# Kernel optimization log

Hardware: AMD Instinct MI355X
Metric: run time of the kernel (lower is better)

The kernel has to match this reference:

```python
import jax, jax.numpy as jnp
import numpy as np

N_NODES = 50000


def gcn_conv(x, W, b, src, dst, n):
    """PyG GCNConv: add self-loops, symmetric deg^-1/2 normalization, then aggregate."""
    loop = jnp.arange(n, dtype=src.dtype)
    s = jnp.concatenate([src, loop])  # [E+N]
    d = jnp.concatenate([dst, loop])  # [E+N]
    deg = jax.ops.segment_sum(jnp.ones_like(d, dtype=x.dtype), d, num_segments=n)  # [N]
    dinv = jnp.where(deg > 0, jax.lax.rsqrt(deg), 0.0)
    h = x @ W  # transform first (reduces message width), [N, out]
    norm = (dinv[s] * dinv[d])[:, None]  # [E+N, 1]
    msgs = h[s] * norm  # gather + scale, [E+N, out]
    out = jax.ops.segment_sum(msgs, d, num_segments=n)  # scatter-add, [N, out]
    return out + b


def setup_inputs() -> dict:
    key = jax.random.key(0)
    k1, k2, k3, k4 = jax.random.split(key, 4)
    in_dim, hidden, n_cls = 512, 256, 64
    x = jax.random.normal(k1, (N_NODES, in_dim), dtype=jnp.float32)
    edge_index = jax.random.randint(k2, (2, 800000), 0, N_NODES, dtype=jnp.int64)
    W1 = jax.random.normal(k3, (in_dim, hidden), dtype=jnp.float32) / np.sqrt(in_dim)
    b1 = jnp.zeros((hidden,), dtype=jnp.float32)
    W2 = jax.random.normal(k4, (hidden, n_cls), dtype=jnp.float32) / np.sqrt(hidden)
    b2 = jnp.zeros((n_cls,), dtype=jnp.float32)
    return {"x": x, "edge_index": edge_index, "W1": W1, "b1": b1, "W2": W2, "b2": b2}


def reference(x, edge_index, W1, b1, W2, b2):
    src, dst = edge_index[0], edge_index[1]
    n = x.shape[0]
    h = jax.nn.relu(gcn_conv(x, W1, b1, src, dst, n))  # dropout is identity in eval mode
    logits = gcn_conv(h, W2, b2, src, dst, n)
    evidence = jax.nn.softplus(logits)
    return (evidence, h)
```

## Files before the change

### kernel.cpp

```cpp
#include <hip/hip_runtime.h>


#define N_NODES 50000
#define IN_DIM 512
#define HID 256
#define NCLS 64

typedef unsigned short u16;
typedef unsigned int u32;
typedef __attribute__((ext_vector_type(8))) short short8;
typedef __attribute__((ext_vector_type(4))) float float4_t;

__device__ __forceinline__ float bf_lo(u32 v) {
    u32 u = v << 16; float f; __builtin_memcpy(&f, &u, 4); return f;
}
__device__ __forceinline__ float bf_hi(u32 v) {
    u32 u = v & 0xffff0000u; float f; __builtin_memcpy(&f, &u, 4); return f;
}
__device__ __forceinline__ u16 f2bf(float f) {
    u32 u; __builtin_memcpy(&u, &f, 4);
    return (u16)((u + 0x7fffu + ((u >> 16) & 1u)) >> 16);
}
__device__ __forceinline__ u32 pk_bf16(float lo, float hi) {
    u32 r;
    asm("v_cvt_pk_bf16_f32 %0, %1, %2" : "=v"(r) : "v"(lo), "v"(hi));
    return r;
}
__device__ __forceinline__ void add8(float* acc, uint4 v) {
    acc[0] += bf_lo(v.x); acc[1] += bf_hi(v.x);
    acc[2] += bf_lo(v.y); acc[3] += bf_hi(v.y);
    acc[4] += bf_lo(v.z); acc[5] += bf_hi(v.z);
    acc[6] += bf_lo(v.w); acc[7] += bf_hi(v.w);
}
__device__ __forceinline__ void acc8(float* acc, uint4 v, float w) {
    acc[0] += w * bf_lo(v.x); acc[1] += w * bf_hi(v.x);
    acc[2] += w * bf_lo(v.y); acc[3] += w * bf_hi(v.y);
    acc[4] += w * bf_lo(v.z); acc[5] += w * bf_hi(v.z);
    acc[6] += w * bf_lo(v.w); acc[7] += w * bf_hi(v.w);
}
__device__ __forceinline__ void nt_store4(float* p, float a, float b, float c, float d) {
    float4_t v = {a, b, c, d};
    __builtin_nontemporal_store(v, (float4_t*)p);
}

__global__ void init_kernel(int* __restrict__ cnt, int* __restrict__ cursor, int n) {
    int i = blockIdx.x * blockDim.x + threadIdx.x;
    if (i < n) { cnt[i] = 0; cursor[i] = 0; }
}

__global__ void count_kernel(const int* __restrict__ dst, int* __restrict__ cnt, int E) {
    int e = blockIdx.x * blockDim.x + threadIdx.x;
    if (e < E) atomicAdd(&cnt[dst[e]], 1);
}

__global__ __launch_bounds__(256) void s1_kernel(const int* __restrict__ cnt,
                                                 int* __restrict__ blocksum,
                                                 float* __restrict__ dinv, int n) {
    int tid = threadIdx.x;
    int i = blockIdx.x * 256 + tid;
    int c = (i < n) ? cnt[i] : 0;
    if (i < n) dinv[i] = rsqrtf((float)(c + 1));
    __shared__ int s[256];
    s[tid] = c;
    __syncthreads();
    for (int off = 128; off > 0; off >>= 1) {
        if (tid < off) s[tid] += s[tid + off];
        __syncthreads();
    }
    if (tid == 0) blocksum[blockIdx.x] = s[0];
}

__global__ __launch_bounds__(256) void s3_kernel(const int* __restrict__ cnt,
                                                 const int* __restrict__ blocksum,
                                                 int* __restrict__ row_ptr, int n, int nb) {
    __shared__ int bs[256];
    __shared__ int s[256];
    int tid = threadIdx.x;
    int v = (tid < nb) ? blocksum[tid] : 0;
    bs[tid] = v;
    __syncthreads();
    for (int off = 1; off < 256; off <<= 1) {
        int a = (tid >= off) ? bs[tid - off] : 0;
        __syncthreads();
        bs[tid] += a;
        __syncthreads();
    }
    int boff = (blockIdx.x == 0) ? 0 : bs[blockIdx.x - 1];
    int i = blockIdx.x * 256 + tid;
    int c = (i < n) ? cnt[i] : 0;
    s[tid] = c;
    __syncthreads();
    for (int off = 1; off < 256; off <<= 1) {
        int a = (tid >= off) ? s[tid - off] : 0;
        __syncthreads();
        s[tid] += a;
        __syncthreads();
    }
    if (i <= n) row_ptr[i] = boff + s[tid] - c;
}

__global__ void fill_kernel(const int* __restrict__ src, const int* __restrict__ dst,
                            const int* __restrict__ row_ptr, int* __restrict__ cursor,
                            int* __restrict__ csr_src, int E) {
    int e = blockIdx.x * blockDim.x + threadIdx.x;
    if (e >= E) return;
    int d = dst[e];
    int pos = row_ptr[d] + atomicAdd(&cursor[d], 1);
    csr_src[pos] = src[e];
}

__global__ __launch_bounds__(256) void tcast2_kernel(const float* __restrict__ W1,
                                                     u16* __restrict__ W1t,
                                                     const float* __restrict__ W2,
                                                     u16* __restrict__ W2t) {
    int idx = blockIdx.x * 256 + threadIdx.x;
    constexpr int N1 = IN_DIM * HID;
    if (idx < N1) {
        int n = idx / IN_DIM, k = idx - n * IN_DIM;
        W1t[idx] = f2bf(W1[k * HID + n]);
    } else {
        int j = idx - N1;
        if (j < HID * NCLS) {
            int n = j / HID, k = j - n * HID;
            W2t[j] = f2bf(W2[k * NCLS + n]);
        }
    }
}

template <int BM, int BN, int K, int N, bool AF32, bool SCALE>
__global__ __launch_bounds__(256) void mfma_gemm_kernel(const void* __restrict__ Ain,
                                                        const u16* __restrict__ Bt,
                                                        u16* __restrict__ C, int M,
                                                        const float* __restrict__ rowscale) {
    constexpr int WROWS = 2, WCOLS = 2;
    constexpr int WMR = BM / WROWS;
    constexpr int WNR = BN / WCOLS;
    constexpr int MR = WMR / 16;
    constexpr int NR = WNR / 16;
    constexpr int AI = BM / 64;
    constexpr int BI = BN / 64;
    constexpr int LDSA = BM * 32;
    constexpr int LDSB = BN * 32;
    constexpr int LDST = LDSA + LDSB;
    constexpr int NT = K / 32;
    static_assert(MR * 16 * WROWS == BM && NR * 16 * WCOLS == BN, "tiling");
    __shared__ u16 lds[2 * LDST];

    const int tid = threadIdx.x;
    const int wave = tid >> 6, lane = tid & 63;
    const int wm = wave / WCOLS, wn = wave % WCOLS;
    const int quad = lane >> 4, l15 = lane & 15;
    const int row0 = blockIdx.y * BM;
    const int col0 = blockIdx.x * BN;

    const float* Af = (const float*)Ain;
    const u16* Abf = (const u16*)Ain;

    int gra[AI];
#pragma unroll
    for (int i = 0; i < AI; i++) {
        int gr = row0 + ((tid + i * 256) >> 2);
        gra[i] = gr < M ? gr : M - 1;
    }

    float4 pa[AI][2];

    auto loadA = [&](int k0) {
#pragma unroll
        for (int i = 0; i < AI; i++) {
            int c = tid + i * 256;
            const float* gp = Af + (long)gra[i] * K + k0 + (c & 3) * 8;
            pa[i][0] = ((const float4*)gp)[0];
            pa[i][1] = ((const float4*)gp)[1];
        }
    };
    auto writeA = [&](u16* buf) {
#pragma unroll
        for (int i = 0; i < AI; i++) {
            int c = tid + i * 256;
            uint4 o;
            o.x = pk_bf16(pa[i][0].x, pa[i][0].y);
            o.y = pk_bf16(pa[i][0].z, pa[i][0].w);
            o.z = pk_bf16(pa[i][1].x, pa[i][1].y);
            o.w = pk_bf16(pa[i][1].z, pa[i][1].w);
            *(uint4*)(buf + c * 8) = o;
        }
    };
    auto stageA_lds = [&](int k0, u16* buf) {
#pragma unroll
        for (int i = 0; i < AI; i++) {
            int c = tid + i * 256;
            const u16* gp = Abf + (long)gra[i] * K + k0 + (c & 3) * 8;
            __builtin_amdgcn_global_load_lds((const __attribute__((address_space(1))) u32*)gp,
                                             (__attribute__((address_space(3))) u32*)(buf + c * 8),
                                             16, 0, 0);
        }
    };
    auto stageB = [&](int k0, u16* buf) {
#pragma unroll
        for (int i = 0; i < BI; i++) {
            int c = tid + i * 256;
            int r = c >> 2;
            const u16* gp = Bt + (long)(col0 + r) * K + k0 + (c & 3) * 8;
            __builtin_amdgcn_global_load_lds((const __attribute__((address_space(1))) u32*)gp,
                                             (__attribute__((address_space(3))) u32*)(buf + c * 8),
                                             16, 0, 0);
        }
    };

    float4_t acc[MR][NR];
#pragma unroll
    for (int mi = 0; mi < MR; mi++)
#pragma unroll
        for (int ni = 0; ni < NR; ni++) {
            float4_t z = {0.f, 0.f, 0.f, 0.f};
            acc[mi][ni] = z;
        }

    if constexpr (AF32) {
        loadA(0);
        writeA(lds);
    } else {
        stageA_lds(0, lds);
    }
    stageB(0, lds + LDSA);
    __syncthreads();

    for (int t = 0; t < NT; t++) {
        u16* cur = lds + (t & 1) * LDST;
        u16* nxt = lds + ((t + 1) & 1) * LDST;
        const bool pre = (t + 1) < NT;
        if (pre) {
            if constexpr (AF32) loadA((t + 1) * 32);
            else stageA_lds((t + 1) * 32, nxt);
            stageB((t + 1) * 32, nxt + LDSA);
        }

        short8 af[MR], bfr[NR];
#pragma unroll
        for (int mi = 0; mi < MR; mi++)
            af[mi] = *(const short8*)(cur + (wm * WMR + mi * 16 + l15) * 32 + quad * 8);
#pragma unroll
        for (int ni = 0; ni < NR; ni++)
            bfr[ni] = *(const short8*)(cur + LDSA + (wn * WNR + ni * 16 + l15) * 32 + quad * 8);
#pragma unroll
        for (int mi = 0; mi < MR; mi++)
#pragma unroll
            for (int ni = 0; ni < NR; ni++)
                acc[mi][ni] = __builtin_amdgcn_mfma_f32_16x16x32_bf16(af[mi], bfr[ni],
                                                                      acc[mi][ni], 0, 0, 0);
        if (pre) {
            if constexpr (AF32) writeA(nxt);
        }
        __syncthreads();
    }

#pragma unroll
    for (int mi = 0; mi < MR; mi++) {
#pragma unroll
        for (int r = 0; r < 4; r++) {
            int row = row0 + wm * WMR + mi * 16 + quad * 4 + r;
            if (row < M) {
                float sc = 1.f;
                if constexpr (SCALE) sc = rowscale[row];
#pragma unroll
                for (int ni = 0; ni < NR; ni++) {
                    int col = col0 + wn * WNR + ni * 16 + l15;
                    C[(long)row * N + col] = f2bf(acc[mi][ni][r] * sc);
                }
            }
        }
    }
}

__global__ __launch_bounds__(256) void agg_wide_kernel(const u16* __restrict__ t,
                                                       const int* __restrict__ row_ptr,
                                                       const int* __restrict__ csr_src,
                                                       const float* __restrict__ dinv,
                                                       const float* __restrict__ bias,
                                                       float* __restrict__ out_f,
                                                       u16* __restrict__ out_bf, int n) {
    constexpr int FEAT = 256;
    int node = (blockIdx.x * blockDim.x + threadIdx.x) >> 6;
    int lane = threadIdx.x & 63;
    if (node >= n) return;
    const int g = lane >> 5;
    const int r = lane & 31;

    const float di = dinv[node];
    uint4 sv = *(const uint4*)(t + (long)node * FEAT + r * 8);
    float4 b0 = *(const float4*)(bias + r * 8);
    float4 b1 = *(const float4*)(bias + r * 8 + 4);

    float acc[8] = {};
    const int beg = row_ptr[node], end = row_ptr[node + 1];
    int e = beg;
    for (; e + 16 <= end; e += 16) {
        int s[8]; uint4 v[8];
#pragma unroll
        for (int u = 0; u < 8; u++) s[u] = csr_src[e + u * 2 + g];
#pragma unroll
        for (int u = 0; u < 8; u++) v[u] = *(const uint4*)(t + (long)s[u] * FEAT + r * 8);
#pragma unroll
        for (int u = 0; u < 8; u++) add8(acc, v[u]);
    }
    for (; e + 8 <= end; e += 8) {
        int s[4]; uint4 v[4];
#pragma unroll
        for (int u = 0; u < 4; u++) s[u] = csr_src[e + u * 2 + g];
#pragma unroll
        for (int u = 0; u < 4; u++) v[u] = *(const uint4*)(t + (long)s[u] * FEAT + r * 8);
#pragma unroll
        for (int u = 0; u < 4; u++) add8(acc, v[u]);
    }
    for (; e < end; e += 2) {
        int ee = e + g;
        if (ee < end) {
            int s = csr_src[ee];
            uint4 v = *(const uint4*)(t + (long)s * FEAT + r * 8);
            add8(acc, v);
        }
    }
#pragma unroll
    for (int j = 0; j < 8; j++) acc[j] += __shfl_xor(acc[j], 32, 64);

    if (lane < 32) {
        float self[8] = {bf_lo(sv.x), bf_hi(sv.x), bf_lo(sv.y), bf_hi(sv.y),
                         bf_lo(sv.z), bf_hi(sv.z), bf_lo(sv.w), bf_hi(sv.w)};
        float bb[8] = {b0.x, b0.y, b0.z, b0.w, b1.x, b1.y, b1.z, b1.w};
        float rv[8];
#pragma unroll
        for (int j = 0; j < 8; j++)
            rv[j] = fmaxf(di * (acc[j] + self[j]) + bb[j], 0.f);
        long base = (long)node * FEAT + lane * 8;
        nt_store4(out_f + base, rv[0], rv[1], rv[2], rv[3]);
        nt_store4(out_f + base + 4, rv[4], rv[5], rv[6], rv[7]);
        uint4 o;
        o.x = pk_bf16(rv[0], rv[1]);
        o.y = pk_bf16(rv[2], rv[3]);
        o.z = pk_bf16(rv[4], rv[5]);
        o.w = pk_bf16(rv[6], rv[7]);
        *(uint4*)(out_bf + base) = o;
    }
}

__global__ __launch_bounds__(256) void agg_n8_kernel(const u16* __restrict__ t,
                                                     const int* __restrict__ row_ptr,
                                                     const int* __restrict__ csr_src,
                                                     const float* __restrict__ dinv,
                                                     const float* __restrict__ bias,
                                                     float* __restrict__ out_f, int n) {
    constexpr int FEAT = 64;
    const int wid = (blockIdx.x * blockDim.x + threadIdx.x) >> 6;
    const int lane = threadIdx.x & 63;
    const int g = lane >> 3;
    const int r = lane & 7;
    const int node = wid * 8 + g;
    const bool valid = node < n;
    const int nd = valid ? node : (n - 1);
    const int beg = row_ptr[nd];
    const int deg = valid ? (row_ptr[nd + 1] - beg) : 0;

    const float di = dinv[nd];
    uint4 sv = *(const uint4*)(t + (long)nd * FEAT + r * 8);
    float4 b0 = *(const float4*)(bias + r * 8);
    float4 b1 = *(const float4*)(bias + r * 8 + 4);

    float acc[8] = {};
    for (int e = 0;; e += 4) {
        if (!__any(e < deg)) break;
        int s[4]; float w[4]; uint4 v[4];
#pragma unroll
        for (int u = 0; u < 4; u++) {
            bool a = (e + u) < deg;
            s[u] = a ? csr_src[beg + e + u] : 0;
            w[u] = a ? 1.f : 0.f;
        }
#pragma unroll
        for (int u = 0; u < 4; u++) v[u] = *(const uint4*)(t + (long)s[u] * FEAT + r * 8);
#pragma unroll
        for (int u = 0; u < 4; u++) acc8(acc, v[u], w[u]);
    }
    float self[8] = {bf_lo(sv.x), bf_hi(sv.x), bf_lo(sv.y), bf_hi(sv.y),
                     bf_lo(sv.z), bf_hi(sv.z), bf_lo(sv.w), bf_hi(sv.w)};
    float bb[8] = {b0.x, b0.y, b0.z, b0.w, b1.x, b1.y, b1.z, b1.w};
    float rv[8];
#pragma unroll
    for (int j = 0; j < 8; j++) {
        float v = di * (acc[j] + self[j]) + bb[j];
        rv[j] = fmaxf(v, 0.f) + __logf(1.f + __expf(-fabsf(v)));
    }
    if (valid) {
        long base = (long)nd * FEAT + r * 8;
        nt_store4(out_f + base, rv[0], rv[1], rv[2], rv[3]);
        nt_store4(out_f + base + 4, rv[4], rv[5], rv[6], rv[7]);
    }
}

extern "C" void kernel_launch(void* const* d_in, const int* in_sizes, int n_in,
                              void* d_out, int out_size, void* d_ws, size_t ws_size,
                              hipStream_t stream) {
    const float* x  = (const float*)d_in[0];
    const int*   ei = (const int*)d_in[1];
    const float* W1 = (const float*)d_in[2];
    const float* b1 = (const float*)d_in[3];
    const float* W2 = (const float*)d_in[4];
    const float* b2 = (const float*)d_in[5];

    float* evidence = (float*)d_out;
    float* h        = (float*)d_out + (long)N_NODES * NCLS;

    const int E = in_sizes[1] / 2;
    const int* src = ei;
    const int* dst = ei + E;

    const int NB = (N_NODES + 255) / 256;

    char* w = (char*)d_ws;
    int*   cnt      = (int*)w;  w += 50048 * 4;
    int*   cursor   = (int*)w;  w += 50048 * 4;
    int*   row_ptr  = (int*)w;  w += 50064 * 4;
    float* dinv     = (float*)w; w += 50048 * 4;
    int*   blocksum = (int*)w;  w += 256 * 4;
    int*   csr_src  = (int*)w;  w += 800000 * 4;
    u16*   hbf      = (u16*)w;  w += (long)N_NODES * IN_DIM * 2;
    u16*   w1t      = (u16*)w;  w += IN_DIM * HID * 2;
    u16*   w2t      = (u16*)w;  w += HID * NCLS * 2;
    u16*   t1bf     = (u16*)w;  w += (long)N_NODES * HID * 2;
    u16*   t2bf     = t1bf;

    init_kernel<<<NB, 256, 0, stream>>>(cnt, cursor, N_NODES);
    count_kernel<<<(E + 255) / 256, 256, 0, stream>>>(dst, cnt, E);
    s1_kernel<<<NB, 256, 0, stream>>>(cnt, blocksum, dinv, N_NODES);
    s3_kernel<<<NB, 256, 0, stream>>>(cnt, blocksum, row_ptr, N_NODES, NB);
    fill_kernel<<<(E + 255) / 256, 256, 0, stream>>>(src, dst, row_ptr, cursor, csr_src, E);

    {
        int tot = IN_DIM * HID + HID * NCLS;
        tcast2_kernel<<<(tot + 255) / 256, 256, 0, stream>>>(W1, w1t, W2, w2t);
    }

    {
        dim3 grid(HID / 64, (N_NODES + 127) / 128);
        mfma_gemm_kernel<128, 64, IN_DIM, HID, true, true>
            <<<grid, 256, 0, stream>>>(x, w1t, t1bf, N_NODES, dinv);
    }
    agg_wide_kernel<<<(N_NODES * 64 + 255) / 256, 256, 0, stream>>>(
        t1bf, row_ptr, csr_src, dinv, b1, h, hbf, N_NODES);

    {
        dim3 grid(NCLS / 64, (N_NODES + 63) / 64);
        mfma_gemm_kernel<64, 64, HID, NCLS, false, true>
            <<<grid, 256, 0, stream>>>(hbf, w2t, t2bf, N_NODES, dinv);
    }
    {
        int waves = (N_NODES + 7) / 8;
        int blocks = (waves + 3) / 4;
        agg_n8_kernel<<<blocks, 256, 0, stream>>>(
            t2bf, row_ptr, csr_src, dinv, b2, evidence, N_NODES);
    }
}
```

Before: 397.6 us.

## Double-buffer neighbor gathers in aggregation kernels and set occupancy launch bounds

Both aggregation kernels now prefetch the next batch of gathered neighbor feature rows into a second register buffer while accumulating the current batch. This is meant to hide gather latency behind the adds. Launch bounds now request 4 blocks per CU to keep occupancy up. The extra buffers raise register pressure and could cause spills under the tighter bound.

```diff
diff --git a/kernel.cpp b/kernel.cpp
--- a/kernel.cpp
+++ b/kernel.cpp
@@ -273,13 +273,13 @@
     }
 }
 
-__global__ __launch_bounds__(256) void agg_wide_kernel(const u16* __restrict__ t,
-                                                       const int* __restrict__ row_ptr,
-                                                       const int* __restrict__ csr_src,
-                                                       const float* __restrict__ dinv,
-                                                       const float* __restrict__ bias,
-                                                       float* __restrict__ out_f,
-                                                       u16* __restrict__ out_bf, int n) {
+__global__ __launch_bounds__(256, 4) void agg_wide_kernel(const u16* __restrict__ t,
+                                                          const int* __restrict__ row_ptr,
+                                                          const int* __restrict__ csr_src,
+                                                          const float* __restrict__ dinv,
+                                                          const float* __restrict__ bias,
+                                                          float* __restrict__ out_f,
+                                                          u16* __restrict__ out_bf, int n) {
     constexpr int FEAT = 256;
     int node = (blockIdx.x * blockDim.x + threadIdx.x) >> 6;
     int lane = threadIdx.x & 63;
@@ -294,15 +294,40 @@
 
     float acc[8] = {};
     const int beg = row_ptr[node], end = row_ptr[node + 1];
+
+    uint4 vA[8], vB[8];
+    auto loadBatch = [&](int eb, uint4* v) {
+        int s[8];
+#pragma unroll
+        for (int u = 0; u < 8; u++) s[u] = csr_src[eb + u * 2 + g];
+#pragma unroll
+        for (int u = 0; u < 8; u++) v[u] = *(const uint4*)(t + (long)s[u] * FEAT + r * 8);
+    };
+
     int e = beg;
-    for (; e + 16 <= end; e += 16) {
-        int s[8]; uint4 v[8];
-#pragma unroll
-        for (int u = 0; u < 8; u++) s[u] = csr_src[e + u * 2 + g];
-#pragma unroll
-        for (int u = 0; u < 8; u++) v[u] = *(const uint4*)(t + (long)s[u] * FEAT + r * 8);
-#pragma unroll
-        for (int u = 0; u < 8; u++) add8(acc, v[u]);
+    const int nb = (end - beg) >> 4;
+    if (nb) loadBatch(e, vA);
+    int i = 1;
+    for (; i + 1 < nb; i += 2) {
+        loadBatch(e + 16, vB);
+#pragma unroll
+        for (int u = 0; u < 8; u++) add8(acc, vA[u]);
+        loadBatch(e + 32, vA);
+#pragma unroll
+        for (int u = 0; u < 8; u++) add8(acc, vB[u]);
+        e += 32;
+    }
+    if (i < nb) {
+        loadBatch(e + 16, vB);
+#pragma unroll
+        for (int u = 0; u < 8; u++) add8(acc, vA[u]);
+#pragma unroll
+        for (int u = 0; u < 8; u++) add8(acc, vB[u]);
+        e += 32;
+    } else if (nb) {
+#pragma unroll
+        for (int u = 0; u < 8; u++) add8(acc, vA[u]);
+        e += 16;
     }
     for (; e + 8 <= end; e += 8) {
         int s[4]; uint4 v[4];
@@ -344,12 +369,12 @@
     }
 }
 
-__global__ __launch_bounds__(256) void agg_n8_kernel(const u16* __restrict__ t,
-                                                     const int* __restrict__ row_ptr,
-                                                     const int* __restrict__ csr_src,
-                                                     const float* __restrict__ dinv,
-                                                     const float* __restrict__ bias,
-                                                     float* __restrict__ out_f, int n) {
+__global__ __launch_bounds__(256, 4) void agg_n8_kernel(const u16* __restrict__ t,
+                                                        const int* __restrict__ row_ptr,
+                                                        const int* __restrict__ csr_src,
+                                                        const float* __restrict__ dinv,
+                                                        const float* __restrict__ bias,
+                                                        float* __restrict__ out_f, int n) {
     constexpr int FEAT = 64;
     const int wid = (blockIdx.x * blockDim.x + threadIdx.x) >> 6;
     const int lane = threadIdx.x & 63;
@@ -367,19 +392,36 @@
     float4 b1 = *(const float4*)(bias + r * 8 + 4);
 
     float acc[8] = {};
-    for (int e = 0;; e += 4) {
-        if (!__any(e < deg)) break;
-        int s[4]; float w[4]; uint4 v[4];
+    uint4 vA[4], vB[4];
+    float wA[4], wB[4];
+    auto loadBatch = [&](int e0, uint4* v, float* w) {
+        int s[4];
 #pragma unroll
         for (int u = 0; u < 4; u++) {
-            bool a = (e + u) < deg;
-            s[u] = a ? csr_src[beg + e + u] : 0;
+            bool a = (e0 + u) < deg;
+            s[u] = a ? csr_src[beg + e0 + u] : 0;
             w[u] = a ? 1.f : 0.f;
         }
 #pragma unroll
         for (int u = 0; u < 4; u++) v[u] = *(const uint4*)(t + (long)s[u] * FEAT + r * 8);
-#pragma unroll
-        for (int u = 0; u < 4; u++) acc8(acc, v[u], w[u]);
+    };
+
+    int e = 0;
+    bool haveA = __any(0 < deg);
+    if (haveA) loadBatch(0, vA, wA);
+    while (haveA) {
+        bool haveB = __any(e + 4 < deg);
+        if (haveB) loadBatch(e + 4, vB, wB);
+#pragma unroll
+        for (int u = 0; u < 4; u++) acc8(acc, vA[u], wA[u]);
+        e += 4;
+        if (!haveB) break;
+        bool haveC = __any(e + 4 < deg);
+        if (haveC) loadBatch(e + 4, vA, wA);
+#pragma unroll
+        for (int u = 0; u < 4; u++) acc8(acc, vB[u], wB[u]);
+        e += 4;
+        haveA = haveC;
     }
     float self[8] = {bf_lo(sv.x), bf_hi(sv.x), bf_lo(sv.y), bf_hi(sv.y),
                      bf_lo(sv.z), bf_hi(sv.z), bf_lo(sv.w), bf_hi(sv.w)};
```

Measured after the change: 421.7 us. +6.1%, slower.
